# Kernel tuning notes

Hardware: AMD Instinct MI355X
Metric: run time of the kernel (lower is better)

The kernel has to match this reference:

```python
import jax, jax.numpy as jnp
import numpy as np

N_NODES = 50000
N_EDGES = 1600000
IN_SIZE = 128
NUM_HEADS = 4
OUT_SIZE = 32


def setup_inputs() -> dict:
    key = jax.random.key(0)
    k1, k2, k3, k4 = jax.random.split(key, 4)
    feat = jax.random.normal(k1, (N_NODES, IN_SIZE), dtype=jnp.float32)
    src = jax.random.randint(k2, (N_EDGES,), 0, N_NODES)
    dst = jnp.sort(jax.random.randint(k3, (N_EDGES,), 0, N_NODES))
    # fc weight of DGL DotGatConv: Linear(in_size, num_heads*out_size, bias=False)
    W = jax.random.normal(k4, (IN_SIZE, NUM_HEADS * OUT_SIZE), dtype=jnp.float32) * 0.05
    return {"feat": feat, "src": src, "dst": dst, "W": W}


def reference(feat, src, dst, W):
    N = feat.shape[0]
    H, D = NUM_HEADS, OUT_SIZE
    # project: [N, H, D]
    h = (feat @ W).reshape(N, H, D)
    h_src = h[src]            # [E, H, D] gather
    h_dst = h[dst]            # [E, H, D] gather
    # per-edge dot-product attention score, scaled by sqrt(out_size)
    e = jnp.sum(h_src * h_dst, axis=-1) / jnp.sqrt(jnp.asarray(D, h.dtype))  # [E, H]
    # edge softmax over incoming edges of each destination node
    m = jax.ops.segment_max(e, dst, num_segments=N)        # [N, H]
    ex = jnp.exp(e - m[dst])                               # [E, H]
    s = jax.ops.segment_sum(ex, dst, num_segments=N)       # [N, H]
    alpha = ex / s[dst]                                    # [E, H]
    # weighted aggregation of source features: sum_e alpha_e * h_src_e -> dst
    out = jax.ops.segment_sum(alpha[:, :, None] * h_src, dst, num_segments=N)  # [N, H, D]
    return out
```

## Files before the change

kernel.cpp:

```cpp
#include <hip/hip_runtime.h>
#include <math.h>

#define N_NODES 50000
#define N_EDGES 1600000
#define IN_SIZE 128
#define HD 128
#define NUM_HEADS 4
#define OUT_SIZE 32
#define STRIPS (N_NODES / 16)
#define STRIPS_PER_WAVE 3
#define PROJ_WAVES ((STRIPS + STRIPS_PER_WAVE - 1) / STRIPS_PER_WAVE)
#define PROJ_BLOCKS ((PROJ_WAVES + 3) / 4)
#define OFF_BLOCKS ((N_NODES + 1 + 255) / 256)

#define SCALE2 0.25503486f

typedef _Float16 half8 __attribute__((ext_vector_type(8)));
typedef _Float16 half2v __attribute__((ext_vector_type(2)));
typedef __attribute__((ext_vector_type(4))) float floatx4;

static __device__ __forceinline__ half2v pk_f16(float a, float b) {
#if __has_builtin(__builtin_amdgcn_cvt_pkrtz)
    auto r = __builtin_amdgcn_cvt_pkrtz(a, b);
    union { decltype(r) i; half2v o; } u;
    u.i = r;
    return u.o;
#else
    half2v r; r.x = (_Float16)a; r.y = (_Float16)b; return r;
#endif
}

static __device__ __forceinline__ float dot2(half2v a, half2v b, float c) {
#if __has_builtin(__builtin_amdgcn_fdot2)
    return __builtin_amdgcn_fdot2(a, b, c, false);
#else
    return fmaf((float)a.x, (float)b.x, fmaf((float)a.y, (float)b.y, c));
#endif
}

static __device__ __forceinline__ half2v shflxor_h2(half2v x, int m) {
    union { half2v h; int i; } u; u.h = x;
    u.i = __shfl_xor(u.i, m);
    return u.h;
}

__global__ __launch_bounds__(256, 1) void k_pre(const float* __restrict__ feat,
                                                const float* __restrict__ W,
                                                const int* __restrict__ dst,
                                                _Float16* __restrict__ hb,
                                                int* __restrict__ off) {
    if (blockIdx.x >= PROJ_BLOCKS) {
        int i = (blockIdx.x - PROJ_BLOCKS) * 256 + threadIdx.x;
        if (i <= N_NODES) {
            int lo = 0, hi = N_EDGES;
            while (lo < hi) {
                int mid = (lo + hi) >> 1;
                if (dst[mid] < i) lo = mid + 1; else hi = mid;
            }
            off[i] = lo;
        }
        return;
    }

    int wid = blockIdx.x * 4 + (threadIdx.x >> 6);
    int lane = threadIdx.x & 63;
    int s0 = wid * STRIPS_PER_WAVE;
    if (s0 >= STRIPS) return;
    int quad = lane >> 4;
    int l15 = lane & 15;

    half8 Bf[8][4];
#pragma unroll
    for (int t = 0; t < 8; t++) {
#pragma unroll
        for (int kb = 0; kb < 4; kb++) {
            union { half8 v; half2v h[4]; } bu;
#pragma unroll
            for (int jj = 0; jj < 4; jj++) {
                int k0 = kb * 32 + quad * 8 + 2 * jj;
                float lo = W[(size_t)k0 * HD + t * 16 + l15];
                float hi = W[(size_t)(k0 + 1) * HD + t * 16 + l15];
                bu.h[jj] = pk_f16(lo, hi);
            }
            Bf[t][kb] = bu.v;
        }
    }

    for (int it = 0; it < STRIPS_PER_WAVE; it++) {
        int strip = s0 + it;
        if (strip >= STRIPS) break;
        int row = strip * 16 + l15;

        const float* ab = feat + (size_t)row * IN_SIZE + quad * 8;
        float4 a[8];
#pragma unroll
        for (int kb = 0; kb < 4; kb++) {
            a[2 * kb]     = *(const float4*)(ab + kb * 32);
            a[2 * kb + 1] = *(const float4*)(ab + kb * 32 + 4);
        }

        floatx4 acc[8];
#pragma unroll
        for (int t = 0; t < 8; t++) acc[t] = (floatx4)(0.f);

#pragma unroll
        for (int kb = 0; kb < 4; kb++) {
            float4 x = a[2 * kb], y = a[2 * kb + 1];
            union { half8 v; half2v h[4]; } af;
            af.h[0] = pk_f16(x.x, x.y);
            af.h[1] = pk_f16(x.z, x.w);
            af.h[2] = pk_f16(y.x, y.y);
            af.h[3] = pk_f16(y.z, y.w);
#pragma unroll
            for (int t = 0; t < 8; t++)
                acc[t] = __builtin_amdgcn_mfma_f32_16x16x32_f16(af.v, Bf[t][kb], acc[t], 0, 0, 0);
        }

#pragma unroll
        for (int t = 0; t < 8; t++) {
#pragma unroll
            for (int r = 0; r < 4; r++) {
                int R = strip * 16 + quad * 4 + r;
                hb[(size_t)R * HD + t * 16 + l15] = (_Float16)acc[t][r];
            }
        }
    }
}

union U8 { uint4 v[2]; half2v h[8]; };

static __device__ __forceinline__ void loadq(U8 (&d)[4], int qb, int e1, int g, int p, int n,
                                             const int* __restrict__ src,
                                             const uint4* __restrict__ h4) {
#pragma unroll
    for (int j = 0; j < 4; j++) {
        int ee = qb + 8 * j + g;
        bool a = ee < e1;
        int sv = src[a ? ee : 0];
        int row = a ? sv : n;
        const uint4* rp = h4 + (size_t)row * 16 + 2 * p;
        d[j].v[0] = rp[0];
        d[j].v[1] = rp[1];
    }
}

static __device__ __forceinline__ void procq(const U8 (&vv)[4], int qb, int e1, int g,
                                             const half2v (&hdc)[8], float& s,
                                             half2v (&acc2)[8]) {
#pragma unroll
    for (int j = 0; j < 4; j++) {
        bool valid = (qb + 8 * j + g) < e1;
        float p0 = dot2(vv[j].h[0], hdc[0], 0.f);
        float p1 = dot2(vv[j].h[1], hdc[1], 0.f);
        p0 = dot2(vv[j].h[2], hdc[2], p0);
        p1 = dot2(vv[j].h[3], hdc[3], p1);
        p0 = dot2(vv[j].h[4], hdc[4], p0);
        p1 = dot2(vv[j].h[5], hdc[5], p1);
        p0 = dot2(vv[j].h[6], hdc[6], p0);
        p1 = dot2(vv[j].h[7], hdc[7], p1);
        float pd = p0 + p1;
        pd += __shfl_xor(pd, 1);
        float w = valid ? __builtin_amdgcn_exp2f(pd) : 0.f;
        s += w;
        half2v wh = pk_f16(w, w);
#pragma unroll
        for (int d = 0; d < 8; d++) acc2[d] += vv[j].h[d] * wh;
    }
}

__global__ __launch_bounds__(256) void k_edge(const _Float16* __restrict__ hb,
                                              const int* __restrict__ src,
                                              const int* __restrict__ off,
                                              float* __restrict__ out) {
    int n = (blockIdx.x * 256 + threadIdx.x) >> 6;
    int lane = threadIdx.x & 63;
    if (n >= N_NODES) return;
    int e0 = off[n], e1 = off[n + 1];

    int g = lane >> 3;
    int p = lane & 7;

    const uint4* h4 = (const uint4*)hb;
    const uint4* hrow = h4 + (size_t)n * 16;
    U8 hdv;
    hdv.v[0] = hrow[2 * p];
    hdv.v[1] = hrow[2 * p + 1];
    half2v hdc[8];
    half2v sc2 = pk_f16(SCALE2, SCALE2);
#pragma unroll
    for (int d = 0; d < 8; d++) hdc[d] = hdv.h[d] * sc2;

    float s = 0.f;
    half2v acc2[8];
#pragma unroll
    for (int d = 0; d < 8; d++) acc2[d] = (half2v)(_Float16)0.f;

    U8 va[4], vb[4];
    loadq(va, e0, e1, g, p, n, src, h4);

    int qb = e0;
    while (qb < e1) {
        loadq(vb, qb + 32, e1, g, p, n, src, h4);
        procq(va, qb, e1, g, hdc, s, acc2);
        qb += 32;
        if (qb >= e1) break;
        loadq(va, qb + 32, e1, g, p, n, src, h4);
        procq(vb, qb, e1, g, hdc, s, acc2);
        qb += 32;
    }

    bool o1 = (g & 1) != 0, o2 = (g & 2) != 0, o4 = (g & 4) != 0;
    half2v r1v[4];
#pragma unroll
    for (int j = 0; j < 4; j++) {
        half2v kp = o1 ? acc2[j + 4] : acc2[j];
        half2v sd = o1 ? acc2[j] : acc2[j + 4];
        r1v[j] = kp + shflxor_h2(sd, 8);
    }
    half2v r2v[2];
#pragma unroll
    for (int j = 0; j < 2; j++) {
        half2v kp = o2 ? r1v[j + 2] : r1v[j];
        half2v sd = o2 ? r1v[j] : r1v[j + 2];
        r2v[j] = kp + shflxor_h2(sd, 16);
    }
    half2v kp3 = o4 ? r2v[1] : r2v[0];
    half2v sd3 = o4 ? r2v[0] : r2v[1];
    half2v fin = kp3 + shflxor_h2(sd3, 32);

    s += __shfl_xor(s, 8); s += __shfl_xor(s, 16); s += __shfl_xor(s, 32);
    float inv = (s > 0.f) ? 1.f / s : 0.f;

    int w = 4 * (g & 1) + 2 * ((g >> 1) & 1) + ((g >> 2) & 1);
    int dim = 16 * p + 2 * w;
    float2 o;
    o.x = (float)fin.x * inv;
    o.y = (float)fin.y * inv;
    *(float2*)(out + (size_t)n * HD + dim) = o;
}

extern "C" void kernel_launch(void* const* d_in, const int* in_sizes, int n_in,
                              void* d_out, int out_size, void* d_ws, size_t ws_size,
                              hipStream_t stream) {
    const float* feat = (const float*)d_in[0];
    const int*   src  = (const int*)d_in[1];
    const int*   dst  = (const int*)d_in[2];
    const float* W    = (const float*)d_in[3];
    float* out = (float*)d_out;

    char* ws = (char*)d_ws;
    _Float16* hb = (_Float16*)ws;
    int* off = (int*)(ws + (size_t)N_NODES * HD * 2);

    k_pre<<<PROJ_BLOCKS + OFF_BLOCKS, 256, 0, stream>>>(feat, W, dst, hb, off);
    k_edge<<<(N_NODES + 3) / 4, 256, 0, stream>>>(hb, src, off, out);
}
```

Baseline: 145.7 us.

## Split projected features into two head-pair halves and run edge kernel twice

The projection now writes h as two planar halves (heads 0-1 and heads 2-3), each 64 halfs per node. The edge kernel processes one half at a time and is launched twice, each launch gathering 128-byte rows instead of 256-byte rows. The aim is to shrink the gathered working set per pass so it fits better in L2/MALL cache. The cost is reading src and off twice, running two launches, and leaving half the lanes idle on the output store.

```diff
diff --git a/kernel.cpp b/kernel.cpp
--- a/kernel.cpp
+++ b/kernel.cpp
@@ -12,6 +12,7 @@
 #define PROJ_WAVES ((STRIPS + STRIPS_PER_WAVE - 1) / STRIPS_PER_WAVE)
 #define PROJ_BLOCKS ((PROJ_WAVES + 3) / 4)
 #define OFF_BLOCKS ((N_NODES + 1 + 255) / 256)
+#define EDGE_BLOCKS ((N_NODES + 3) / 4)
 
 #define SCALE2 0.25503486f
 
@@ -121,32 +122,32 @@
 #pragma unroll
             for (int r = 0; r < 4; r++) {
                 int R = strip * 16 + quad * 4 + r;
-                hb[(size_t)R * HD + t * 16 + l15] = (_Float16)acc[t][r];
+                size_t addr = (size_t)(t >> 2) * ((size_t)N_NODES * 64)
+                            + (size_t)R * 64 + (t & 3) * 16 + l15;
+                hb[addr] = (_Float16)acc[t][r];
             }
         }
     }
 }
 
-union U8 { uint4 v[2]; half2v h[8]; };
-
-static __device__ __forceinline__ void loadq(U8 (&d)[4], int qb, int e1, int g, int p, int n,
+union U4 { uint4 v; half2v h[4]; };
+
+static __device__ __forceinline__ void loadq(U4 (&d)[4], int qb, int e1, int g, int p, int n,
                                              const int* __restrict__ src,
-                                             const uint4* __restrict__ h4) {
+                                             const uint4* __restrict__ h4h) {
 #pragma unroll
     for (int j = 0; j < 4; j++) {
         int ee = qb + 8 * j + g;
         bool a = ee < e1;
         int sv = src[a ? ee : 0];
         int row = a ? sv : n;
-        const uint4* rp = h4 + (size_t)row * 16 + 2 * p;
-        d[j].v[0] = rp[0];
-        d[j].v[1] = rp[1];
-    }
-}
-
-static __device__ __forceinline__ void procq(const U8 (&vv)[4], int qb, int e1, int g,
-                                             const half2v (&hdc)[8], float& s,
-                                             half2v (&acc2)[8]) {
+        d[j].v = h4h[(size_t)row * 8 + p];
+    }
+}
+
+static __device__ __forceinline__ void procq(const U4 (&vv)[4], int qb, int e1, int g,
+                                             const half2v (&hdc)[4], float& s,
+                                             half2v (&acc2)[4]) {
 #pragma unroll
     for (int j = 0; j < 4; j++) {
         bool valid = (qb + 8 * j + g) < e1;
@@ -154,24 +155,21 @@
         float p1 = dot2(vv[j].h[1], hdc[1], 0.f);
         p0 = dot2(vv[j].h[2], hdc[2], p0);
         p1 = dot2(vv[j].h[3], hdc[3], p1);
-        p0 = dot2(vv[j].h[4], hdc[4], p0);
-        p1 = dot2(vv[j].h[5], hdc[5], p1);
-        p0 = dot2(vv[j].h[6], hdc[6], p0);
-        p1 = dot2(vv[j].h[7], hdc[7], p1);
         float pd = p0 + p1;
         pd += __shfl_xor(pd, 1);
+        pd += __shfl_xor(pd, 2);
         float w = valid ? __builtin_amdgcn_exp2f(pd) : 0.f;
         s += w;
         half2v wh = pk_f16(w, w);
 #pragma unroll
-        for (int d = 0; d < 8; d++) acc2[d] += vv[j].h[d] * wh;
-    }
-}
-
-__global__ __launch_bounds__(256) void k_edge(const _Float16* __restrict__ hb,
+        for (int d = 0; d < 4; d++) acc2[d] += vv[j].h[d] * wh;
+    }
+}
+
+__global__ __launch_bounds__(256) void k_edge(const _Float16* __restrict__ hbh,
                                               const int* __restrict__ src,
                                               const int* __restrict__ off,
-                                              float* __restrict__ out) {
+                                              float* __restrict__ outh) {
     int n = (blockIdx.x * 256 + threadIdx.x) >> 6;
     int lane = threadIdx.x & 63;
     if (n >= N_NODES) return;
@@ -180,63 +178,56 @@
     int g = lane >> 3;
     int p = lane & 7;
 
-    const uint4* h4 = (const uint4*)hb;
-    const uint4* hrow = h4 + (size_t)n * 16;
-    U8 hdv;
-    hdv.v[0] = hrow[2 * p];
-    hdv.v[1] = hrow[2 * p + 1];
-    half2v hdc[8];
+    const uint4* h4h = (const uint4*)hbh;
+    U4 hdv;
+    hdv.v = h4h[(size_t)n * 8 + p];
+    half2v hdc[4];
     half2v sc2 = pk_f16(SCALE2, SCALE2);
 #pragma unroll
-    for (int d = 0; d < 8; d++) hdc[d] = hdv.h[d] * sc2;
+    for (int d = 0; d < 4; d++) hdc[d] = hdv.h[d] * sc2;
 
     float s = 0.f;
-    half2v acc2[8];
-#pragma unroll
-    for (int d = 0; d < 8; d++) acc2[d] = (half2v)(_Float16)0.f;
-
-    U8 va[4], vb[4];
-    loadq(va, e0, e1, g, p, n, src, h4);
+    half2v acc2[4];
+#pragma unroll
+    for (int d = 0; d < 4; d++) acc2[d] = (half2v)(_Float16)0.f;
+
+    U4 va[4], vb[4];
+    loadq(va, e0, e1, g, p, n, src, h4h);
 
     int qb = e0;
     while (qb < e1) {
-        loadq(vb, qb + 32, e1, g, p, n, src, h4);
+        loadq(vb, qb + 32, e1, g, p, n, src, h4h);
         procq(va, qb, e1, g, hdc, s, acc2);
         qb += 32;
         if (qb >= e1) break;
-        loadq(va, qb + 32, e1, g, p, n, src, h4);
+        loadq(va, qb + 32, e1, g, p, n, src, h4h);
         procq(vb, qb, e1, g, hdc, s, acc2);
         qb += 32;
     }
 
-    bool o1 = (g & 1) != 0, o2 = (g & 2) != 0, o4 = (g & 4) != 0;
-    half2v r1v[4];
-#pragma unroll
-    for (int j = 0; j < 4; j++) {
-        half2v kp = o1 ? acc2[j + 4] : acc2[j];
-        half2v sd = o1 ? acc2[j] : acc2[j + 4];
-        r1v[j] = kp + shflxor_h2(sd, 8);
-    }
-    half2v r2v[2];
-#pragma unroll
-    for (int j = 0; j < 2; j++) {
-        half2v kp = o2 ? r1v[j + 2] : r1v[j];
-        half2v sd = o2 ? r1v[j] : r1v[j + 2];
-        r2v[j] = kp + shflxor_h2(sd, 16);
-    }
-    half2v kp3 = o4 ? r2v[1] : r2v[0];
-    half2v sd3 = o4 ? r2v[0] : r2v[1];
-    half2v fin = kp3 + shflxor_h2(sd3, 32);
+    bool o1 = (g & 1) != 0, o2 = (g & 2) != 0;
+    half2v t0 = o1 ? acc2[2] : acc2[0];
+    half2v t1 = o1 ? acc2[3] : acc2[1];
+    half2v s0 = o1 ? acc2[0] : acc2[2];
+    half2v s1 = o1 ? acc2[1] : acc2[3];
+    t0 = t0 + shflxor_h2(s0, 8);
+    t1 = t1 + shflxor_h2(s1, 8);
+    half2v k2 = o2 ? t1 : t0;
+    half2v s2 = o2 ? t0 : t1;
+    k2 = k2 + shflxor_h2(s2, 16);
+    half2v fin = k2 + shflxor_h2(k2, 32);
 
     s += __shfl_xor(s, 8); s += __shfl_xor(s, 16); s += __shfl_xor(s, 32);
     float inv = (s > 0.f) ? 1.f / s : 0.f;
 
-    int w = 4 * (g & 1) + 2 * ((g >> 1) & 1) + ((g >> 2) & 1);
-    int dim = 16 * p + 2 * w;
-    float2 o;
-    o.x = (float)fin.x * inv;
-    o.y = (float)fin.y * inv;
-    *(float2*)(out + (size_t)n * HD + dim) = o;
+    if (g < 4) {
+        int w = 2 * (g & 1) + ((g >> 1) & 1);
+        int dim = 8 * p + 2 * w;
+        float2 o;
+        o.x = (float)fin.x * inv;
+        o.y = (float)fin.y * inv;
+        *(float2*)(outh + (size_t)n * HD + dim) = o;
+    }
 }
 
 extern "C" void kernel_launch(void* const* d_in, const int* in_sizes, int n_in,
@@ -253,5 +244,6 @@
     int* off = (int*)(ws + (size_t)N_NODES * HD * 2);
 
     k_pre<<<PROJ_BLOCKS + OFF_BLOCKS, 256, 0, stream>>>(feat, W, dst, hb, off);
-    k_edge<<<(N_NODES + 3) / 4, 256, 0, stream>>>(hb, src, off, out);
-}
+    k_edge<<<EDGE_BLOCKS, 256, 0, stream>>>(hb, src, off, out);
+    k_edge<<<EDGE_BLOCKS, 256, 0, stream>>>(hb + (size_t)N_NODES * 64, src, off, out + 64);
+}
```

New measurement: 148.2 us. Within noise of the previous version (+1.7%).
